# Kernel optimization log

Measured on AMD Instinct MI355X. Metric: run time of the kernel, lower is better.

The kernel has to match this reference:

```python
import jax, jax.numpy as jnp
import numpy as np

L = 8        # num_coupling
W = 128      # MLP hidden width
B = 262144   # batch size


def _lin(k, out_d, in_d):
    # torch nn.Linear default init: U(-1/sqrt(in_d), 1/sqrt(in_d))
    scale = 1.0 / np.sqrt(in_d)
    kw, kb = jax.random.split(k)
    Wm = jax.random.uniform(kw, (L, out_d, in_d), minval=-scale, maxval=scale, dtype=jnp.float32)
    bm = jax.random.uniform(kb, (L, out_d), minval=-scale, maxval=scale, dtype=jnp.float32)
    return Wm, bm


def setup_inputs() -> dict:
    key = jax.random.key(0)
    ks = jax.random.split(key, 10)
    x = jax.random.normal(ks[0], (B, 2), dtype=jnp.float32)
    s_scale = jax.random.normal(ks[1], (L,), dtype=jnp.float32)
    s_W1, s_b1 = _lin(ks[2], W, 1)
    s_W2, s_b2 = _lin(ks[3], W, W)
    s_W3, s_b3 = _lin(ks[4], W, W)
    s_W4, s_b4 = _lin(ks[5], 1, W)
    t_W1, t_b1 = _lin(ks[6], W, 1)
    t_W2, t_b2 = _lin(ks[7], W, W)
    t_W3, t_b3 = _lin(ks[8], W, W)
    t_W4, t_b4 = _lin(ks[9], 1, W)
    return dict(x=x, s_scale=s_scale,
                s_W1=s_W1, s_b1=s_b1, s_W2=s_W2, s_b2=s_b2, s_W3=s_W3, s_b3=s_b3, s_W4=s_W4, s_b4=s_b4,
                t_W1=t_W1, t_b1=t_b1, t_W2=t_W2, t_b2=t_b2, t_W3=t_W3, t_b3=t_b3, t_W4=t_W4, t_b4=t_b4)


def _mlp(z, W1, b1, W2, b2, W3, b3, W4, b4):
    # backbone: Linear->ReLU x3, Linear->Tanh; z: [B,1] -> [B,1]
    h = jax.nn.relu(z @ W1.T + b1)
    h = jax.nn.relu(h @ W2.T + b2)
    h = jax.nn.relu(h @ W3.T + b3)
    return jnp.tanh(h @ W4.T + b4)


def reference(x, s_scale,
              s_W1, s_b1, s_W2, s_b2, s_W3, s_b3, s_W4, s_b4,
              t_W1, t_b1, t_W2, t_b2, t_W3, t_b3, t_W4, t_b4):
    # training-mode forward of NormalizingFlow2D
    a = x[:, :1]
    b = x[:, 1:]
    s_vals = []
    for i in range(L):
        if i % 2 == 0:
            s = s_scale[i] * _mlp(a, s_W1[i], s_b1[i], s_W2[i], s_b2[i], s_W3[i], s_b3[i], s_W4[i], s_b4[i])
            b = jnp.exp(s) * b + _mlp(a, t_W1[i], t_b1[i], t_W2[i], t_b2[i], t_W3[i], t_b3[i], t_W4[i], t_b4[i])
        else:
            s = s_scale[i] * _mlp(b, s_W1[i], s_b1[i], s_W2[i], s_b2[i], s_W3[i], s_b3[i], s_W4[i], s_b4[i])
            a = jnp.exp(s) * a + _mlp(b, t_W1[i], t_b1[i], t_W2[i], t_b2[i], t_W3[i], t_b3[i], t_W4[i], t_b4[i])
        s_vals.append(s)
    out = jnp.concatenate([a, b], axis=1)          # [B, 2]
    s_cat = jnp.concatenate(s_vals, axis=0)        # [L*B, 1]  (torch.cat default dim=0)
    return out, s_cat
```

## Files before the change

kernel.cpp:

```cpp
#include <hip/hip_runtime.h>

#define LNUM 8
#define WD 128
#define BATCH 262144

typedef unsigned int u32;
typedef __attribute__((ext_vector_type(8))) short bf16x8;
typedef __attribute__((ext_vector_type(4))) float f32x4;

__device__ __forceinline__ u32 pk2(float x, float y){
  u32 r;
  asm("v_cvt_pk_bf16_f32 %0, %1, %2" : "=v"(r) : "v"(x), "v"(y));
  return r;
}

__device__ __forceinline__ void stage_Wnat(const float* __restrict__ src, u32* dst, int tid){
  const int j = tid >> 1, h = tid & 1;
  const float* s = src + j * WD + h * 64;
  u32* drow = dst + j * 64;
  const int base = h * 32;
  const u32 sz = (u32)((j & 7) << 2);
#pragma unroll
  for(int c = 0; c < 8; ++c){
    float4 f0 = *(const float4*)(s + c * 8);
    float4 f1 = *(const float4*)(s + c * 8 + 4);
    uint4 w;
    w.x = pk2(f0.x, f0.y); w.y = pk2(f0.z, f0.w);
    w.z = pk2(f1.x, f1.y); w.w = pk2(f1.z, f1.w);
    *(uint4*)(drow + (((u32)(base + c * 4)) ^ sz)) = w;
  }
}

__device__ __forceinline__ void stage_Wperm(const float* __restrict__ src, u32* dst, int tid){
  const int j = tid >> 1, h = tid & 1;
  const float* srow = src + j * WD;
  u32* drow = dst + j * 64;
  const u32 sz = (u32)((j & 7) << 2);
#pragma unroll
  for(int kk = 0; kk < 2; ++kk){
    const int kt = 2 * h + kk;
#pragma unroll
    for(int g = 0; g < 4; ++g){
      float4 f0 = *(const float4*)(srow + kt * 32 + g * 4);
      float4 f1 = *(const float4*)(srow + kt * 32 + 16 + g * 4);
      uint4 w;
      w.x = pk2(f0.x, f0.y); w.y = pk2(f0.z, f0.w);
      w.z = pk2(f1.x, f1.y); w.w = pk2(f1.z, f1.w);
      *(uint4*)(drow + (((u32)(kt * 16 + g * 4)) ^ sz)) = w;
    }
  }
}

__device__ __forceinline__ void stage_dma(const u32* __restrict__ g, u32* l, int wv, int lane){
#pragma unroll
  for(int it = 0; it < 8; ++it){
    const int o = wv * 2048 + it * 256;
    __builtin_amdgcn_global_load_lds(
        (const __attribute__((address_space(1))) u32*)(g + o + lane * 4),
        (__attribute__((address_space(3))) u32*)(l + o),
        16, 0, 0);
  }
}

#define PACK_ST(dstv, uv) do { \
    uint4 pk_; \
    pk_.x = pk2(fmaxf(fmaf(uv, w1a_.x, g1a_.x), 0.f), fmaxf(fmaf(uv, w1a_.y, g1a_.y), 0.f)); \
    pk_.y = pk2(fmaxf(fmaf(uv, w1a_.z, g1a_.z), 0.f), fmaxf(fmaf(uv, w1a_.w, g1a_.w), 0.f)); \
    pk_.z = pk2(fmaxf(fmaf(uv, w1b_.x, g1b_.x), 0.f), fmaxf(fmaf(uv, w1b_.y, g1b_.y), 0.f)); \
    pk_.w = pk2(fmaxf(fmaf(uv, w1b_.z, g1b_.z), 0.f), fmaxf(fmaf(uv, w1b_.w, g1b_.w), 0.f)); \
    dstv = __builtin_bit_cast(bf16x8, pk_); \
  } while(0)

#define PACK_BV(buf, ktc) do { \
    const int ko_ = (ktc) * 32 + lg * 8; \
    const float4 w1a_ = *(const float4*)(W1 + ko_); \
    const float4 w1b_ = *(const float4*)(W1 + ko_ + 4); \
    const float4 g1a_ = *(const float4*)(b1 + ko_); \
    const float4 g1b_ = *(const float4*)(b1 + ko_ + 4); \
    PACK_ST((buf)[0], us0); PACK_ST((buf)[1], us1); \
    PACK_ST((buf)[2], us2); PACK_ST((buf)[3], us3); \
  } while(0)

#define FOLD(jtc) do { \
    const float4 wc_ = *(const float4*)(W4 + (jtc) * 16 + lg * 4); \
    p0 = fmaf(fmaxf(aa[(jtc)&1][0][0], 0.f), wc_.x, p0); \
    p0 = fmaf(fmaxf(aa[(jtc)&1][0][1], 0.f), wc_.y, p0); \
    p0 = fmaf(fmaxf(aa[(jtc)&1][0][2], 0.f), wc_.z, p0); \
    p0 = fmaf(fmaxf(aa[(jtc)&1][0][3], 0.f), wc_.w, p0); \
    p1 = fmaf(fmaxf(aa[(jtc)&1][1][0], 0.f), wc_.x, p1); \
    p1 = fmaf(fmaxf(aa[(jtc)&1][1][1], 0.f), wc_.y, p1); \
    p1 = fmaf(fmaxf(aa[(jtc)&1][1][2], 0.f), wc_.z, p1); \
    p1 = fmaf(fmaxf(aa[(jtc)&1][1][3], 0.f), wc_.w, p1); \
    p2 = fmaf(fmaxf(aa[(jtc)&1][2][0], 0.f), wc_.x, p2); \
    p2 = fmaf(fmaxf(aa[(jtc)&1][2][1], 0.f), wc_.y, p2); \
    p2 = fmaf(fmaxf(aa[(jtc)&1][2][2], 0.f), wc_.z, p2); \
    p2 = fmaf(fmaxf(aa[(jtc)&1][2][3], 0.f), wc_.w, p2); \
    p3 = fmaf(fmaxf(aa[(jtc)&1][3][0], 0.f), wc_.x, p3); \
    p3 = fmaf(fmaxf(aa[(jtc)&1][3][1], 0.f), wc_.y, p3); \
    p3 = fmaf(fmaxf(aa[(jtc)&1][3][2], 0.f), wc_.z, p3); \
    p3 = fmaf(fmaxf(aa[(jtc)&1][3][3], 0.f), wc_.w, p3); \
  } while(0)

__device__ __forceinline__ float mlp_full(
    float u, const u32* __restrict__ W2lds, const u32* __restrict__ W3lds,
    const float* __restrict__ W1, const float* __restrict__ b1,
    const float* __restrict__ b2, const float* __restrict__ b3,
    const float* __restrict__ W4, int lm, int lg)
{
  const float us0 = __shfl(u, lm, 64);
  const float us1 = __shfl(u, 16 + lm, 64);
  const float us2 = __shfl(u, 32 + lm, 64);
  const float us3 = __shfl(u, 48 + lm, 64);

  f32x4 acc1[8][4];
#pragma unroll
  for(int jt = 0; jt < 8; ++jt){
    const float4 bb = *(const float4*)(b2 + jt * 16 + lg * 4);
    const f32x4 binit = {bb.x, bb.y, bb.z, bb.w};
#pragma unroll
    for(int st = 0; st < 4; ++st) acc1[jt][st] = binit;
  }

  bf16x8 bv[2][4];
  PACK_BV(bv[0], 0);
#pragma unroll
  for(int kt = 0; kt < 4; ++kt){
    if(kt < 3) PACK_BV(bv[(kt + 1) & 1], kt + 1);
    const u32 kdw = (u32)(kt * 16 + lg * 4);
    __builtin_amdgcn_s_setprio(1);
#pragma unroll
    for(int jt = 0; jt < 8; ++jt){
      const int j = lm + 16 * jt;
      bf16x8 av = __builtin_bit_cast(bf16x8,
          *(const uint4*)(W2lds + j * 64 + (kdw ^ (u32)((j & 7) << 2))));
#pragma unroll
      for(int st = 0; st < 4; ++st)
        acc1[jt][st] = __builtin_amdgcn_mfma_f32_16x16x32_bf16(av, bv[kt & 1][st], acc1[jt][st], 0, 0, 0);
    }
    __builtin_amdgcn_s_setprio(0);
  }

  uint4 trq[4][4];
#pragma unroll
  for(int jt = 0; jt < 8; ++jt)
#pragma unroll
    for(int st = 0; st < 4; ++st){
      const u32 d0 = pk2(fmaxf(acc1[jt][st][0], 0.f), fmaxf(acc1[jt][st][1], 0.f));
      const u32 d1 = pk2(fmaxf(acc1[jt][st][2], 0.f), fmaxf(acc1[jt][st][3], 0.f));
      if(jt & 1){ trq[jt >> 1][st].z = d0; trq[jt >> 1][st].w = d1; }
      else      { trq[jt >> 1][st].x = d0; trq[jt >> 1][st].y = d1; }
    }

  f32x4 aa[2][4];
  float p0 = 0.f, p1 = 0.f, p2 = 0.f, p3 = 0.f;
#pragma unroll
  for(int jt = 0; jt < 8; ++jt){
    const int j = lm + 16 * jt;
    const u32 sz = (u32)((j & 7) << 2);
    const u32* r = W3lds + j * 64;
    bf16x8 av[4];
#pragma unroll
    for(int kt = 0; kt < 4; ++kt)
      av[kt] = __builtin_bit_cast(bf16x8,
          *(const uint4*)(r + (((u32)(kt * 16 + lg * 4)) ^ sz)));
    const float4 bc = *(const float4*)(b3 + jt * 16 + lg * 4);
    const f32x4 cinit = {bc.x, bc.y, bc.z, bc.w};
#pragma unroll
    for(int st = 0; st < 4; ++st) aa[jt & 1][st] = cinit;
    if(jt > 0) FOLD(jt - 1);
    __builtin_amdgcn_s_setprio(1);
#pragma unroll
    for(int kt = 0; kt < 4; ++kt)
#pragma unroll
      for(int st = 0; st < 4; ++st)
        aa[jt & 1][st] = __builtin_amdgcn_mfma_f32_16x16x32_bf16(
            av[kt], __builtin_bit_cast(bf16x8, trq[kt][st]), aa[jt & 1][st], 0, 0, 0);
    __builtin_amdgcn_s_setprio(0);
  }
  FOLD(7);

  p0 += __shfl_xor(p0, 16, 64); p0 += __shfl_xor(p0, 32, 64);
  p1 += __shfl_xor(p1, 16, 64); p1 += __shfl_xor(p1, 32, 64);
  p2 += __shfl_xor(p2, 16, 64); p2 += __shfl_xor(p2, 32, 64);
  p3 += __shfl_xor(p3, 16, 64); p3 += __shfl_xor(p3, 32, 64);
  return (lg == 0) ? p0 : (lg == 1) ? p1 : (lg == 2) ? p2 : p3;
}

extern "C" __global__ void __launch_bounds__(256)
prep_kernel(const float* __restrict__ sW2, const float* __restrict__ sW3,
            const float* __restrict__ tW2, const float* __restrict__ tW3,
            u32* __restrict__ ws)
{
  const int b = blockIdx.x;
  const int layer = b >> 2, which = b & 3;
  const float* src = (which == 0 ? sW2 : which == 1 ? sW3 : which == 2 ? tW2 : tW3)
                     + layer * (WD * WD);
  u32* dst = ws + b * 8192;
  if(which & 1) stage_Wperm(src, dst, threadIdx.x);
  else          stage_Wnat (src, dst, threadIdx.x);
}

extern "C" __global__ void __launch_bounds__(512)
flow_dma(const float* __restrict__ x, const float* __restrict__ s_scale,
         const float* __restrict__ sW1, const float* __restrict__ sb1,
         const float* __restrict__ sb2, const float* __restrict__ sb3,
         const float* __restrict__ sW4, const float* __restrict__ sb4,
         const float* __restrict__ tW1, const float* __restrict__ tb1,
         const float* __restrict__ tb2, const float* __restrict__ tb3,
         const float* __restrict__ tW4, const float* __restrict__ tb4,
         const u32* __restrict__ wimg, float* __restrict__ out)
{
  __shared__ u32 Wbuf[2][16384];

  const int tid = threadIdx.x;
  const int lane = tid & 63, lg = lane >> 4, lm = lane & 15, wv = tid >> 6;
  const int gs = (int)blockIdx.x * 512 + tid;

  float2 ab = ((const float2*)x)[gs];
  float* scat = out + 2 * BATCH;
  float sv = 0.f;

  stage_dma(wimg, Wbuf[0], wv, lane);

#pragma unroll 1
  for(int ph = 0; ph < 2 * LNUM; ++ph){
    const int i = ph >> 1, isT = ph & 1, parity = i & 1;
    asm volatile("s_waitcnt vmcnt(0)" ::: "memory");
    __syncthreads();
    if(ph < 2 * LNUM - 1)
      stage_dma(wimg + (ph + 1) * 16384, Wbuf[(ph + 1) & 1], wv, lane);

    const int off = i * WD;
    const float u = parity ? ab.y : ab.x;
    const u32* W2l = Wbuf[ph & 1];
    const u32* W3l = Wbuf[ph & 1] + 8192;

    if(!isT){
      float pre = mlp_full(u, W2l, W3l, sW1 + off, sb1 + off,
                           sb2 + off, sb3 + off, sW4 + off, lm, lg) + sb4[i];
      sv = s_scale[i] * tanhf(pre);
      scat[i * BATCH + gs] = sv;
    } else {
      float pre = mlp_full(u, W2l, W3l, tW1 + off, tb1 + off,
                           tb2 + off, tb3 + off, tW4 + off, lm, lg) + tb4[i];
      const float tv = tanhf(pre);
      const float e = expf(sv);
      if(parity) ab.x = e * ab.x + tv; else ab.y = e * ab.y + tv;
    }
  }

  ((float2*)out)[gs] = ab;
}

extern "C" __global__ void __launch_bounds__(256, 2)
flow_fb(const float* __restrict__ x, const float* __restrict__ s_scale,
        const float* __restrict__ sW1, const float* __restrict__ sb1,
        const float* __restrict__ sW2, const float* __restrict__ sb2,
        const float* __restrict__ sW3, const float* __restrict__ sb3,
        const float* __restrict__ sW4, const float* __restrict__ sb4,
        const float* __restrict__ tW1, const float* __restrict__ tb1,
        const float* __restrict__ tW2, const float* __restrict__ tb2,
        const float* __restrict__ tW3, const float* __restrict__ tb3,
        const float* __restrict__ tW4, const float* __restrict__ tb4,
        float* __restrict__ out)
{
  __shared__ u32 Wlds[2][8192];

  const int tid = threadIdx.x;
  const int lane = tid & 63, lg = lane >> 4, lm = lane & 15;
  const int gs = (int)blockIdx.x * 256 + tid;

  float2 ab = ((const float2*)x)[gs];
  float* scat = out + 2 * BATCH;

#pragma unroll 1
  for(int i = 0; i < LNUM; ++i){
    const int parity = i & 1;
    const float sc = s_scale[i];
    const int off = i * WD, offW = i * (WD * WD);

    __syncthreads();
    stage_Wnat (sW2 + offW, Wlds[0], tid);
    stage_Wperm(sW3 + offW, Wlds[1], tid);
    __syncthreads();
    const float u = parity ? ab.y : ab.x;
    float preS = mlp_full(u, Wlds[0], Wlds[1], sW1 + off, sb1 + off,
                          sb2 + off, sb3 + off, sW4 + off, lm, lg) + sb4[i];
    const float sv = sc * tanhf(preS);
    scat[i * BATCH + gs] = sv;

    __syncthreads();
    stage_Wnat (tW2 + offW, Wlds[0], tid);
    stage_Wperm(tW3 + offW, Wlds[1], tid);
    __syncthreads();
    float preT = mlp_full(u, Wlds[0], Wlds[1], tW1 + off, tb1 + off,
                          tb2 + off, tb3 + off, tW4 + off, lm, lg) + tb4[i];
    const float tv = tanhf(preT);
    const float e = expf(sv);
    if(parity) ab.x = e * ab.x + tv; else ab.y = e * ab.y + tv;
  }

  ((float2*)out)[gs] = ab;
}

extern "C" void kernel_launch(void* const* d_in, const int* in_sizes, int n_in,
                              void* d_out, int out_size, void* d_ws, size_t ws_size,
                              hipStream_t stream) {
  (void)in_sizes; (void)n_in; (void)out_size;
  const float* p[18];
  for(int k = 0; k < 18; ++k) p[k] = (const float*)d_in[k];

  const size_t need = (size_t)32 * 8192 * 4;
  if(ws_size >= need){
    u32* ws = (u32*)d_ws;
    hipLaunchKernelGGL(prep_kernel, dim3(32), dim3(256), 0, stream,
                       p[4], p[6], p[12], p[14], ws);
    hipLaunchKernelGGL(flow_dma, dim3(BATCH / 512), dim3(512), 0, stream,
                       p[0], p[1], p[2], p[3], p[5], p[7], p[8], p[9],
                       p[10], p[11], p[13], p[15], p[16], p[17],
                       (const u32*)ws, (float*)d_out);
  } else {
    hipLaunchKernelGGL(flow_fb, dim3(BATCH / 256), dim3(256), 0, stream,
                       p[0], p[1], p[2], p[3], p[4], p[5], p[6], p[7], p[8], p[9],
                       p[10], p[11], p[12], p[13], p[14], p[15], p[16], p[17],
                       (float*)d_out);
  }
}
```

Baseline: 274.1 us.

## Halve samples per wavefront to cut accumulator registers and double block size

Each wavefront now processes 32 samples instead of 64, using two MFMA column tiles instead of four, and the first layer is split into two passes of four output tiles to shrink live accumulators. Blocks grow to 1024 threads with a matching smaller per-wave DMA slice, so each block still covers 512 samples. The aim is lower VGPR pressure and higher occupancy to better hide LDS and MFMA latency. In exchange, half the lanes carry redundant work in the input shuffle and epilogue, and the ratio of weight loads to MFMAs doubles.

```diff
diff --git a/kernel.cpp b/kernel.cpp
--- a/kernel.cpp
+++ b/kernel.cpp
@@ -51,10 +51,20 @@
   }
 }
 
-__device__ __forceinline__ void stage_dma(const u32* __restrict__ g, u32* l, int wv, int lane){
-#pragma unroll
-  for(int it = 0; it < 8; ++it){
-    const int o = wv * 2048 + it * 256;
+__device__ __forceinline__ void stage_dma16(const u32* __restrict__ g, u32* l, int wv, int lane){
+#pragma unroll
+  for(int it = 0; it < 4; ++it){
+    const int o = wv * 1024 + it * 256;
+    __builtin_amdgcn_global_load_lds(
+        (const __attribute__((address_space(1))) u32*)(g + o + lane * 4),
+        (__attribute__((address_space(3))) u32*)(l + o),
+        16, 0, 0);
+  }
+}
+__device__ __forceinline__ void stage_dma4(const u32* __restrict__ g, u32* l, int wv, int lane){
+#pragma unroll
+  for(int it = 0; it < 16; ++it){
+    const int o = wv * 4096 + it * 256;
     __builtin_amdgcn_global_load_lds(
         (const __attribute__((address_space(1))) u32*)(g + o + lane * 4),
         (__attribute__((address_space(3))) u32*)(l + o),
@@ -71,17 +81,7 @@
     dstv = __builtin_bit_cast(bf16x8, pk_); \
   } while(0)
 
-#define PACK_BV(buf, ktc) do { \
-    const int ko_ = (ktc) * 32 + lg * 8; \
-    const float4 w1a_ = *(const float4*)(W1 + ko_); \
-    const float4 w1b_ = *(const float4*)(W1 + ko_ + 4); \
-    const float4 g1a_ = *(const float4*)(b1 + ko_); \
-    const float4 g1b_ = *(const float4*)(b1 + ko_ + 4); \
-    PACK_ST((buf)[0], us0); PACK_ST((buf)[1], us1); \
-    PACK_ST((buf)[2], us2); PACK_ST((buf)[3], us3); \
-  } while(0)
-
-#define FOLD(jtc) do { \
+#define FOLD2(jtc) do { \
     const float4 wc_ = *(const float4*)(W4 + (jtc) * 16 + lg * 4); \
     p0 = fmaf(fmaxf(aa[(jtc)&1][0][0], 0.f), wc_.x, p0); \
     p0 = fmaf(fmaxf(aa[(jtc)&1][0][1], 0.f), wc_.y, p0); \
@@ -91,68 +91,68 @@
     p1 = fmaf(fmaxf(aa[(jtc)&1][1][1], 0.f), wc_.y, p1); \
     p1 = fmaf(fmaxf(aa[(jtc)&1][1][2], 0.f), wc_.z, p1); \
     p1 = fmaf(fmaxf(aa[(jtc)&1][1][3], 0.f), wc_.w, p1); \
-    p2 = fmaf(fmaxf(aa[(jtc)&1][2][0], 0.f), wc_.x, p2); \
-    p2 = fmaf(fmaxf(aa[(jtc)&1][2][1], 0.f), wc_.y, p2); \
-    p2 = fmaf(fmaxf(aa[(jtc)&1][2][2], 0.f), wc_.z, p2); \
-    p2 = fmaf(fmaxf(aa[(jtc)&1][2][3], 0.f), wc_.w, p2); \
-    p3 = fmaf(fmaxf(aa[(jtc)&1][3][0], 0.f), wc_.x, p3); \
-    p3 = fmaf(fmaxf(aa[(jtc)&1][3][1], 0.f), wc_.y, p3); \
-    p3 = fmaf(fmaxf(aa[(jtc)&1][3][2], 0.f), wc_.z, p3); \
-    p3 = fmaf(fmaxf(aa[(jtc)&1][3][3], 0.f), wc_.w, p3); \
   } while(0)
 
-__device__ __forceinline__ float mlp_full(
+__device__ __forceinline__ float mlp32(
     float u, const u32* __restrict__ W2lds, const u32* __restrict__ W3lds,
     const float* __restrict__ W1, const float* __restrict__ b1,
     const float* __restrict__ b2, const float* __restrict__ b3,
-    const float* __restrict__ W4, int lm, int lg)
+    const float* __restrict__ W4, int lm, int lg, int lane)
 {
   const float us0 = __shfl(u, lm, 64);
   const float us1 = __shfl(u, 16 + lm, 64);
-  const float us2 = __shfl(u, 32 + lm, 64);
-  const float us3 = __shfl(u, 48 + lm, 64);
-
-  f32x4 acc1[8][4];
-#pragma unroll
-  for(int jt = 0; jt < 8; ++jt){
-    const float4 bb = *(const float4*)(b2 + jt * 16 + lg * 4);
-    const f32x4 binit = {bb.x, bb.y, bb.z, bb.w};
-#pragma unroll
-    for(int st = 0; st < 4; ++st) acc1[jt][st] = binit;
-  }
-
-  bf16x8 bv[2][4];
-  PACK_BV(bv[0], 0);
+
+  bf16x8 bv[4][2];
 #pragma unroll
   for(int kt = 0; kt < 4; ++kt){
-    if(kt < 3) PACK_BV(bv[(kt + 1) & 1], kt + 1);
-    const u32 kdw = (u32)(kt * 16 + lg * 4);
+    const int ko_ = kt * 32 + lg * 8;
+    const float4 w1a_ = *(const float4*)(W1 + ko_);
+    const float4 w1b_ = *(const float4*)(W1 + ko_ + 4);
+    const float4 g1a_ = *(const float4*)(b1 + ko_);
+    const float4 g1b_ = *(const float4*)(b1 + ko_ + 4);
+    PACK_ST(bv[kt][0], us0);
+    PACK_ST(bv[kt][1], us1);
+  }
+
+  uint4 trq[4][2];
+#pragma unroll
+  for(int jb = 0; jb < 2; ++jb){
+    f32x4 acc[4][2];
+#pragma unroll
+    for(int q = 0; q < 4; ++q){
+      const float4 bb = *(const float4*)(b2 + (jb * 4 + q) * 16 + lg * 4);
+      const f32x4 bi = {bb.x, bb.y, bb.z, bb.w};
+      acc[q][0] = bi; acc[q][1] = bi;
+    }
     __builtin_amdgcn_s_setprio(1);
 #pragma unroll
-    for(int jt = 0; jt < 8; ++jt){
-      const int j = lm + 16 * jt;
-      bf16x8 av = __builtin_bit_cast(bf16x8,
-          *(const uint4*)(W2lds + j * 64 + (kdw ^ (u32)((j & 7) << 2))));
-#pragma unroll
-      for(int st = 0; st < 4; ++st)
-        acc1[jt][st] = __builtin_amdgcn_mfma_f32_16x16x32_bf16(av, bv[kt & 1][st], acc1[jt][st], 0, 0, 0);
+    for(int kt = 0; kt < 4; ++kt){
+      const u32 kdw = (u32)(kt * 16 + lg * 4);
+#pragma unroll
+      for(int q = 0; q < 4; ++q){
+        const int j = lm + 16 * (jb * 4 + q);
+        bf16x8 av = __builtin_bit_cast(bf16x8,
+            *(const uint4*)(W2lds + j * 64 + (kdw ^ (u32)((j & 7) << 2))));
+        acc[q][0] = __builtin_amdgcn_mfma_f32_16x16x32_bf16(av, bv[kt][0], acc[q][0], 0, 0, 0);
+        acc[q][1] = __builtin_amdgcn_mfma_f32_16x16x32_bf16(av, bv[kt][1], acc[q][1], 0, 0, 0);
+      }
     }
     __builtin_amdgcn_s_setprio(0);
-  }
-
-  uint4 trq[4][4];
-#pragma unroll
-  for(int jt = 0; jt < 8; ++jt)
-#pragma unroll
-    for(int st = 0; st < 4; ++st){
-      const u32 d0 = pk2(fmaxf(acc1[jt][st][0], 0.f), fmaxf(acc1[jt][st][1], 0.f));
-      const u32 d1 = pk2(fmaxf(acc1[jt][st][2], 0.f), fmaxf(acc1[jt][st][3], 0.f));
-      if(jt & 1){ trq[jt >> 1][st].z = d0; trq[jt >> 1][st].w = d1; }
-      else      { trq[jt >> 1][st].x = d0; trq[jt >> 1][st].y = d1; }
-    }
-
-  f32x4 aa[2][4];
-  float p0 = 0.f, p1 = 0.f, p2 = 0.f, p3 = 0.f;
+#pragma unroll
+    for(int q = 0; q < 4; ++q){
+      const int jt = jb * 4 + q;
+#pragma unroll
+      for(int st = 0; st < 2; ++st){
+        const u32 d0 = pk2(fmaxf(acc[q][st][0], 0.f), fmaxf(acc[q][st][1], 0.f));
+        const u32 d1 = pk2(fmaxf(acc[q][st][2], 0.f), fmaxf(acc[q][st][3], 0.f));
+        if(jt & 1){ trq[jt >> 1][st].z = d0; trq[jt >> 1][st].w = d1; }
+        else      { trq[jt >> 1][st].x = d0; trq[jt >> 1][st].y = d1; }
+      }
+    }
+  }
+
+  f32x4 aa[2][2];
+  float p0 = 0.f, p1 = 0.f;
 #pragma unroll
   for(int jt = 0; jt < 8; ++jt){
     const int j = lm + 16 * jt;
@@ -164,26 +164,24 @@
       av[kt] = __builtin_bit_cast(bf16x8,
           *(const uint4*)(r + (((u32)(kt * 16 + lg * 4)) ^ sz)));
     const float4 bc = *(const float4*)(b3 + jt * 16 + lg * 4);
-    const f32x4 cinit = {bc.x, bc.y, bc.z, bc.w};
-#pragma unroll
-    for(int st = 0; st < 4; ++st) aa[jt & 1][st] = cinit;
-    if(jt > 0) FOLD(jt - 1);
+    const f32x4 ci = {bc.x, bc.y, bc.z, bc.w};
+    aa[jt & 1][0] = ci; aa[jt & 1][1] = ci;
+    if(jt > 0) FOLD2(jt - 1);
     __builtin_amdgcn_s_setprio(1);
 #pragma unroll
-    for(int kt = 0; kt < 4; ++kt)
-#pragma unroll
-      for(int st = 0; st < 4; ++st)
-        aa[jt & 1][st] = __builtin_amdgcn_mfma_f32_16x16x32_bf16(
-            av[kt], __builtin_bit_cast(bf16x8, trq[kt][st]), aa[jt & 1][st], 0, 0, 0);
+    for(int kt = 0; kt < 4; ++kt){
+      aa[jt & 1][0] = __builtin_amdgcn_mfma_f32_16x16x32_bf16(
+          av[kt], __builtin_bit_cast(bf16x8, trq[kt][0]), aa[jt & 1][0], 0, 0, 0);
+      aa[jt & 1][1] = __builtin_amdgcn_mfma_f32_16x16x32_bf16(
+          av[kt], __builtin_bit_cast(bf16x8, trq[kt][1]), aa[jt & 1][1], 0, 0, 0);
+    }
     __builtin_amdgcn_s_setprio(0);
   }
-  FOLD(7);
+  FOLD2(7);
 
   p0 += __shfl_xor(p0, 16, 64); p0 += __shfl_xor(p0, 32, 64);
   p1 += __shfl_xor(p1, 16, 64); p1 += __shfl_xor(p1, 32, 64);
-  p2 += __shfl_xor(p2, 16, 64); p2 += __shfl_xor(p2, 32, 64);
-  p3 += __shfl_xor(p3, 16, 64); p3 += __shfl_xor(p3, 32, 64);
-  return (lg == 0) ? p0 : (lg == 1) ? p1 : (lg == 2) ? p2 : p3;
+  return (lane & 16) ? p1 : p0;
 }
 
 extern "C" __global__ void __launch_bounds__(256)
@@ -200,7 +198,7 @@
   else          stage_Wnat (src, dst, threadIdx.x);
 }
 
-extern "C" __global__ void __launch_bounds__(512)
+extern "C" __global__ void __launch_bounds__(1024)
 flow_dma(const float* __restrict__ x, const float* __restrict__ s_scale,
          const float* __restrict__ sW1, const float* __restrict__ sb1,
          const float* __restrict__ sb2, const float* __restrict__ sb3,
@@ -214,13 +212,15 @@
 
   const int tid = threadIdx.x;
   const int lane = tid & 63, lg = lane >> 4, lm = lane & 15, wv = tid >> 6;
-  const int gs = (int)blockIdx.x * 512 + tid;
-
-  float2 ab = ((const float2*)x)[gs];
+  const int sBase = (int)blockIdx.x * 512 + wv * 32;
+  const bool owner = (lane < 32);
+
+  float2 ab = make_float2(0.f, 0.f);
+  if(owner) ab = ((const float2*)x)[sBase + lane];
   float* scat = out + 2 * BATCH;
   float sv = 0.f;
 
-  stage_dma(wimg, Wbuf[0], wv, lane);
+  stage_dma16(wimg, Wbuf[0], wv, lane);
 
 #pragma unroll 1
   for(int ph = 0; ph < 2 * LNUM; ++ph){
@@ -228,7 +228,7 @@
     asm volatile("s_waitcnt vmcnt(0)" ::: "memory");
     __syncthreads();
     if(ph < 2 * LNUM - 1)
-      stage_dma(wimg + (ph + 1) * 16384, Wbuf[(ph + 1) & 1], wv, lane);
+      stage_dma16(wimg + (ph + 1) * 16384, Wbuf[(ph + 1) & 1], wv, lane);
 
     const int off = i * WD;
     const float u = parity ? ab.y : ab.x;
@@ -236,23 +236,23 @@
     const u32* W3l = Wbuf[ph & 1] + 8192;
 
     if(!isT){
-      float pre = mlp_full(u, W2l, W3l, sW1 + off, sb1 + off,
-                           sb2 + off, sb3 + off, sW4 + off, lm, lg) + sb4[i];
+      float pre = mlp32(u, W2l, W3l, sW1 + off, sb1 + off,
+                        sb2 + off, sb3 + off, sW4 + off, lm, lg, lane) + sb4[i];
       sv = s_scale[i] * tanhf(pre);
-      scat[i * BATCH + gs] = sv;
+      if(owner) scat[i * BATCH + sBase + lane] = sv;
     } else {
-      float pre = mlp_full(u, W2l, W3l, tW1 + off, tb1 + off,
-                           tb2 + off, tb3 + off, tW4 + off, lm, lg) + tb4[i];
+      float pre = mlp32(u, W2l, W3l, tW1 + off, tb1 + off,
+                        tb2 + off, tb3 + off, tW4 + off, lm, lg, lane) + tb4[i];
       const float tv = tanhf(pre);
       const float e = expf(sv);
       if(parity) ab.x = e * ab.x + tv; else ab.y = e * ab.y + tv;
     }
   }
 
-  ((float2*)out)[gs] = ab;
-}
-
-extern "C" __global__ void __launch_bounds__(256, 2)
+  if(owner) ((float2*)out)[sBase + lane] = ab;
+}
+
+extern "C" __global__ void __launch_bounds__(256)
 flow_fb(const float* __restrict__ x, const float* __restrict__ s_scale,
         const float* __restrict__ sW1, const float* __restrict__ sb1,
         const float* __restrict__ sW2, const float* __restrict__ sb2,
@@ -267,16 +267,18 @@
   __shared__ u32 Wlds[2][8192];
 
   const int tid = threadIdx.x;
-  const int lane = tid & 63, lg = lane >> 4, lm = lane & 15;
-  const int gs = (int)blockIdx.x * 256 + tid;
-
-  float2 ab = ((const float2*)x)[gs];
+  const int lane = tid & 63, lg = lane >> 4, lm = lane & 15, wv = tid >> 6;
+  const int sBase = (int)blockIdx.x * 128 + wv * 32;
+  const bool owner = (lane < 32);
+
+  float2 ab = make_float2(0.f, 0.f);
+  if(owner) ab = ((const float2*)x)[sBase + lane];
   float* scat = out + 2 * BATCH;
+  float sv = 0.f;
 
 #pragma unroll 1
   for(int i = 0; i < LNUM; ++i){
     const int parity = i & 1;
-    const float sc = s_scale[i];
     const int off = i * WD, offW = i * (WD * WD);
 
     __syncthreads();
@@ -284,23 +286,23 @@
     stage_Wperm(sW3 + offW, Wlds[1], tid);
     __syncthreads();
     const float u = parity ? ab.y : ab.x;
-    float preS = mlp_full(u, Wlds[0], Wlds[1], sW1 + off, sb1 + off,
-                          sb2 + off, sb3 + off, sW4 + off, lm, lg) + sb4[i];
-    const float sv = sc * tanhf(preS);
-    scat[i * BATCH + gs] = sv;
+    float preS = mlp32(u, Wlds[0], Wlds[1], sW1 + off, sb1 + off,
+                       sb2 + off, sb3 + off, sW4 + off, lm, lg, lane) + sb4[i];
+    sv = s_scale[i] * tanhf(preS);
+    if(owner) scat[i * BATCH + sBase + lane] = sv;
 
     __syncthreads();
     stage_Wnat (tW2 + offW, Wlds[0], tid);
     stage_Wperm(tW3 + offW, Wlds[1], tid);
     __syncthreads();
-    float preT = mlp_full(u, Wlds[0], Wlds[1], tW1 + off, tb1 + off,
-                          tb2 + off, tb3 + off, tW4 + off, lm, lg) + tb4[i];
+    float preT = mlp32(u, Wlds[0], Wlds[1], tW1 + off, tb1 + off,
+                       tb2 + off, tb3 + off, tW4 + off, lm, lg, lane) + tb4[i];
     const float tv = tanhf(preT);
     const float e = expf(sv);
     if(parity) ab.x = e * ab.x + tv; else ab.y = e * ab.y + tv;
   }
 
-  ((float2*)out)[gs] = ab;
+  if(owner) ((float2*)out)[sBase + lane] = ab;
 }
 
 extern "C" void kernel_launch(void* const* d_in, const int* in_sizes, int n_in,
@@ -315,12 +317,12 @@
     u32* ws = (u32*)d_ws;
     hipLaunchKernelGGL(prep_kernel, dim3(32), dim3(256), 0, stream,
                        p[4], p[6], p[12], p[14], ws);
-    hipLaunchKernelGGL(flow_dma, dim3(BATCH / 512), dim3(512), 0, stream,
+    hipLaunchKernelGGL(flow_dma, dim3(BATCH / 512), dim3(1024), 0, stream,
                        p[0], p[1], p[2], p[3], p[5], p[7], p[8], p[9],
                        p[10], p[11], p[13], p[15], p[16], p[17],
                        (const u32*)ws, (float*)d_out);
   } else {
-    hipLaunchKernelGGL(flow_fb, dim3(BATCH / 256), dim3(256), 0, stream,
+    hipLaunchKernelGGL(flow_fb, dim3(BATCH / 128), dim3(256), 0, stream,
                        p[0], p[1], p[2], p[3], p[4], p[5], p[6], p[7], p[8], p[9],
                        p[10], p[11], p[12], p[13], p[14], p[15], p[16], p[17],
                        (float*)d_out);
```

Result: slower. 608.2 us (+121.9%).
